# Optimization experiments

Hardware: AMD Instinct MI355X
Metric: run time of the kernel (lower is better)

Reference implementation:

```python
import jax, jax.numpy as jnp
import numpy as np

B, S, D = 4, 1024, 4096
HQ, HKV, HD = 32, 8, 128
N_REP = HQ // HKV


def _rope(x, cos, sin):
    # x: [b, s, h, hd]; cos/sin: [s, hd//2]; pairs are (x[..., 2i], x[..., 2i+1])
    xr = x[..., 0::2]
    xi = x[..., 1::2]
    c = cos[None, :, None, :]
    s = sin[None, :, None, :]
    out_r = xr * c - xi * s
    out_i = xr * s + xi * c
    return jnp.stack([out_r, out_i], axis=-1).reshape(x.shape)


def setup_inputs() -> dict:
    key = jax.random.key(0)
    ks = jax.random.split(key, 6)
    x = jax.random.normal(ks[0], (B, S, D), dtype=jnp.float32)
    wq = jax.random.normal(ks[1], (HQ * HD, D), dtype=jnp.float32) * 0.02
    wk = jax.random.normal(ks[2], (HKV * HD, D), dtype=jnp.float32) * 0.02
    wv = jax.random.normal(ks[3], (HKV * HD, D), dtype=jnp.float32) * 0.02
    wo = jax.random.normal(ks[4], (D, HQ * HD), dtype=jnp.float32) * 0.02
    # standard rotary frequencies, theta=10000
    inv_freq = 1.0 / (10000.0 ** (np.arange(0, HD, 2, dtype=np.float32) / HD))
    angles = np.outer(np.arange(S, dtype=np.float32), inv_freq)  # [S, HD//2]
    freqs_cos = jnp.asarray(np.cos(angles), dtype=jnp.float32)
    freqs_sin = jnp.asarray(np.sin(angles), dtype=jnp.float32)
    cache_k = jnp.zeros((B, S, HKV, HD), dtype=jnp.float32)
    cache_v = jnp.zeros((B, S, HKV, HD), dtype=jnp.float32)
    return {"x": x, "wq": wq, "wk": wk, "wv": wv, "wo": wo,
            "freqs_cos": freqs_cos, "freqs_sin": freqs_sin,
            "cache_k": cache_k, "cache_v": cache_v, "start_pos": 0}


def reference(x, wq, wk, wv, wo, freqs_cos, freqs_sin, cache_k, cache_v, start_pos):
    b, s, _ = x.shape
    xq = jnp.einsum('bsd,od->bso', x, wq).reshape(b, s, HQ, HD)
    xk = jnp.einsum('bsd,od->bso', x, wk).reshape(b, s, HKV, HD)
    xv = jnp.einsum('bsd,od->bso', x, wv).reshape(b, s, HKV, HD)
    xq = _rope(xq, freqs_cos, freqs_sin)
    xk = _rope(xk, freqs_cos, freqs_sin)
    # KV-cache append (intended semantics: store keys/values)
    cache_k = jax.lax.dynamic_update_slice(cache_k, xk, (0, start_pos, 0, 0))
    cache_v = jax.lax.dynamic_update_slice(cache_v, xv, (0, start_pos, 0, 0))
    keys = cache_k[:, :start_pos + s]      # [b, kv, HKV, HD]
    values = cache_v[:, :start_pos + s]
    # GQA repeat_kv -> [b, kv, HQ, HD]
    keys = jnp.repeat(keys, N_REP, axis=2)
    values = jnp.repeat(values, N_REP, axis=2)
    scores = jnp.einsum('bqhd,bkhd->bhqk', xq, keys) / jnp.sqrt(jnp.float32(HD))
    probs = jax.nn.softmax(scores.astype(jnp.float32), axis=-1).astype(xq.dtype)
    out = jnp.einsum('bhqk,bkhd->bqhd', probs, values).reshape(b, s, HQ * HD)
    return jnp.einsum('bso,do->bsd', out, wo)
```

## Files before the change

kernel.cpp:

```cpp
#include <hip/hip_runtime.h>

typedef __bf16 bf16_t;
typedef __bf16 bf16x8 __attribute__((ext_vector_type(8)));
typedef __bf16 bf16x4 __attribute__((ext_vector_type(4)));
typedef float  f32x4  __attribute__((ext_vector_type(4)));
typedef short  s16x4  __attribute__((ext_vector_type(4)));

#define SEQ    1024
#define DMODEL 4096
#define NHQ    32
#define NHKV   8
#define HDIM   128

#define GLOAD_LDS16(g, l)                                                  \
    __builtin_amdgcn_global_load_lds(                                      \
        (const __attribute__((address_space(1))) unsigned int*)(g),        \
        (__attribute__((address_space(3))) unsigned int*)(l), 16, 0, 0)

__global__ __launch_bounds__(256)
void f2b(const float* __restrict__ in, bf16_t* __restrict__ out, int n8)
{
    int i = blockIdx.x * 256 + threadIdx.x;
    if (i >= n8) return;
    const float4* p = (const float4*)in + 2 * (size_t)i;
    float4 a = p[0], b = p[1];
    bf16x8 o;
    o[0] = (bf16_t)a.x; o[1] = (bf16_t)a.y; o[2] = (bf16_t)a.z; o[3] = (bf16_t)a.w;
    o[4] = (bf16_t)b.x; o[5] = (bf16_t)b.y; o[6] = (bf16_t)b.z; o[7] = (bf16_t)b.w;
    *((bf16x8*)out + i) = o;
}

#define STAGE_A(b, ks)  do {                                               \
    const char* as_ = Ab + (size_t)srow * Krb + (ks) + scol0;              \
    GLOAD_LDS16(as_,             ldsA[b] + t * 16);                        \
    GLOAD_LDS16(as_ + 128 * Krb, ldsA[b] + 8192 + t * 16);                 \
} while (0)
#define STAGE_B(b, ks)  do {                                               \
    const char* bs_ = Bb + (size_t)srow * Krb + (ks) + scol0;              \
    GLOAD_LDS16(bs_,             ldsB[b] + t * 16);                        \
    GLOAD_LDS16(bs_ + 128 * Krb, ldsB[b] + 8192 + t * 16);                 \
} while (0)
#define LDS_AT(buf, row, lg_) \
    (*(const bf16x8*)((buf) + (row) * 64 + (((lg_) * 16) ^ ((((row) >> 1) & 3) << 4))))

#define TILE(bufi, tno)  do {                                              \
    const int ks3_ = ((tno) + 3 < NT) ? ((tno) + 3) * 64 : 0;              \
      \
    bf16x8 af[8], bfr0, bfr1;                                              \
    _Pragma("unroll")                                                      \
    for (int m = 0; m < 8; ++m) {                                          \
        int row = wm * 128 + m * 16 + l15;                                 \
        af[m] = LDS_AT(ldsA[bufi], row, lg);                               \
    }                                                                      \
    { int rb = wn * 64 + l15;      bfr0 = LDS_AT(ldsB[bufi], rb, lg); }    \
    { int rb = wn * 64 + 16 + l15; bfr1 = LDS_AT(ldsB[bufi], rb, lg); }    \
    STAGE_A(((tno) + 3) & 3, ks3_);                                        \
    __builtin_amdgcn_sched_barrier(0);                                     \
    __builtin_amdgcn_s_barrier();                                          \
    asm volatile("s_waitcnt lgkmcnt(0)" ::: "memory");                     \
    __builtin_amdgcn_sched_barrier(0);                                     \
    __builtin_amdgcn_s_setprio(1);                                         \
    _Pragma("unroll")                                                      \
    for (int m = 0; m < 8; ++m) {                                          \
        acc[m][0] = __builtin_amdgcn_mfma_f32_16x16x32_bf16(af[m], bfr0, acc[m][0], 0, 0, 0); \
        acc[m][1] = __builtin_amdgcn_mfma_f32_16x16x32_bf16(af[m], bfr1, acc[m][1], 0, 0, 0); \
    }                                                                      \
    __builtin_amdgcn_s_setprio(0);                                         \
    __builtin_amdgcn_sched_barrier(0);                                     \
    __builtin_amdgcn_s_barrier();                                          \
       \
    { int rb = wn * 64 + 32 + l15; bfr0 = LDS_AT(ldsB[bufi], rb, lg); }    \
    { int rb = wn * 64 + 48 + l15; bfr1 = LDS_AT(ldsB[bufi], rb, lg); }    \
    STAGE_B(((tno) + 3) & 3, ks3_);                                        \
    __builtin_amdgcn_sched_barrier(0);                                     \
    __builtin_amdgcn_s_barrier();                                          \
    asm volatile("s_waitcnt lgkmcnt(0)" ::: "memory");                     \
    __builtin_amdgcn_sched_barrier(0);                                     \
    __builtin_amdgcn_s_setprio(1);                                         \
    _Pragma("unroll")                                                      \
    for (int m = 0; m < 8; ++m) {                                          \
        acc[m][2] = __builtin_amdgcn_mfma_f32_16x16x32_bf16(af[m], bfr0, acc[m][2], 0, 0, 0); \
        acc[m][3] = __builtin_amdgcn_mfma_f32_16x16x32_bf16(af[m], bfr1, acc[m][3], 0, 0, 0); \
    }                                                                      \
    __builtin_amdgcn_s_setprio(0);                                         \
    asm volatile("s_waitcnt vmcnt(8)" ::: "memory");                       \
    __builtin_amdgcn_sched_barrier(0);                                     \
    __builtin_amdgcn_s_barrier();                                          \
} while (0)

template<bool OUT_F32>
__global__ __launch_bounds__(512, 2)
void gemm256(const bf16_t* __restrict__ A, const bf16_t* __restrict__ B,
             void* __restrict__ Cv, int M, int N, int K, int nbn)
{
    __shared__ __align__(16) char ldsA[4][16384];
    __shared__ __align__(16) char ldsB[4][16384];

    const int nwg = gridDim.x;
    const int bid0 = blockIdx.x;
    const int bid = (bid0 & 7) * (nwg >> 3) + (bid0 >> 3);
    const int bm = bid / nbn, bn = bid % nbn;
    const int t = threadIdx.x;
    const int lane = t & 63, wid = t >> 6;
    const int wm = wid >> 2, wn = wid & 3;
    const int l15 = lane & 15, lg = lane >> 4;
    const int m0 = bm * 256, n0 = bn * 256;

    const int srow = t >> 2;
    const int scol0 = (((t & 3) ^ ((srow >> 1) & 3)) << 4);
    const int Krb = K * 2;
    const char* Ab = (const char*)A + (size_t)m0 * Krb;
    const char* Bb = (const char*)B + (size_t)n0 * Krb;

    const int NT = K >> 5;
    f32x4 acc[8][4] = {};

    STAGE_A(0, 0);   STAGE_B(0, 0);
    STAGE_A(1, 64);  STAGE_B(1, 64);
    STAGE_A(2, 128); STAGE_B(2, 128);
    asm volatile("s_waitcnt vmcnt(8)" ::: "memory");
    __builtin_amdgcn_sched_barrier(0);
    __builtin_amdgcn_s_barrier();

    for (int tt = 0; tt < NT; tt += 4) {
        TILE(0, tt + 0);
        TILE(1, tt + 1);
        TILE(2, tt + 2);
        TILE(3, tt + 3);
    }

    #pragma unroll
    for (int m = 0; m < 8; ++m) {
        int row0 = m0 + wm * 128 + m * 16 + lg * 4;
        #pragma unroll
        for (int n = 0; n < 4; ++n) {
            int col = n0 + wn * 64 + n * 16 + l15;
            #pragma unroll
            for (int i = 0; i < 4; ++i) {
                if constexpr (OUT_F32)
                    ((float*)Cv)[(size_t)(row0 + i) * N + col] = acc[m][n][i];
                else
                    ((bf16_t*)Cv)[(size_t)(row0 + i) * N + col] = (bf16_t)acc[m][n][i];
            }
        }
    }
}
#undef TILE
#undef LDS_AT
#undef STAGE_A
#undef STAGE_B

template<int MODE>
__global__ __launch_bounds__(256, 4)
void gemm_bt(const bf16_t* __restrict__ A, const bf16_t* __restrict__ B,
             void* __restrict__ Cv, bf16_t* __restrict__ Vt,
             int M, int N, int K, int nbn)
{
    __shared__ __align__(16) bf16_t lA[128 * 32];
    __shared__ __align__(16) bf16_t lB[128 * 32];

    const int nwg = gridDim.x;
    const int bid0 = blockIdx.x;
    const int bid = (bid0 & 7) * (nwg >> 3) + (bid0 >> 3);
    const int bm = bid / nbn, bn = bid % nbn;
    const int t = threadIdx.x;
    const int lane = t & 63, wid = t >> 6;
    const int wrow = (wid >> 1) * 64, wcol = (wid & 1) * 64;
    const int l15 = lane & 15, lg = lane >> 4;
    const int m0 = bm * 128, n0 = bn * 128;

    const int r0 = t >> 2, pos0 = (t & 3) * 8;
    const int r1 = r0 + 64;

    const bf16_t* Ar0 = A + (size_t)(m0 + r0) * K + pos0;
    const bf16_t* Ar1 = A + (size_t)(m0 + r1) * K + pos0;
    const bf16_t* Br0 = B + (size_t)(n0 + r0) * K + pos0;
    const bf16_t* Br1 = B + (size_t)(n0 + r1) * K + pos0;

    f32x4 acc[4][4] = {};

    for (int k0 = 0; k0 < K; k0 += 32) {
        __syncthreads();
        GLOAD_LDS16(Ar0 + k0, lA + t * 8);
        GLOAD_LDS16(Ar1 + k0, lA + (t + 256) * 8);
        GLOAD_LDS16(Br0 + k0, lB + t * 8);
        GLOAD_LDS16(Br1 + k0, lB + (t + 256) * 8);
        __syncthreads();

        bf16x8 af[4], bfr[4];
        #pragma unroll
        for (int m = 0; m < 4; ++m)
            af[m] = *(const bf16x8*)(lA + (wrow + m * 16 + l15) * 32 + lg * 8);
        #pragma unroll
        for (int n = 0; n < 4; ++n)
            bfr[n] = *(const bf16x8*)(lB + (wcol + n * 16 + l15) * 32 + lg * 8);
        #pragma unroll
        for (int m = 0; m < 4; ++m)
            #pragma unroll
            for (int n = 0; n < 4; ++n)
                acc[m][n] = __builtin_amdgcn_mfma_f32_16x16x32_bf16(
                    af[m], bfr[n], acc[m][n], 0, 0, 0);
    }

    #pragma unroll
    for (int m = 0; m < 4; ++m) {
        #pragma unroll
        for (int n = 0; n < 4; ++n) {
            int col  = n0 + wcol + n * 16 + l15;
            int row0 = m0 + wrow + m * 16 + lg * 4;
            if constexpr (MODE == 0) {
                #pragma unroll
                for (int i = 0; i < 4; ++i)
                    ((bf16_t*)Cv)[(size_t)(row0 + i) * N + col] = (bf16_t)acc[m][n][i];
            } else if constexpr (MODE == 1) {
                #pragma unroll
                for (int i = 0; i < 4; ++i)
                    ((float*)Cv)[(size_t)(row0 + i) * N + col] = acc[m][n][i];
            } else {
                if (col < 1024) {
                    #pragma unroll
                    for (int i = 0; i < 4; ++i)
                        ((bf16_t*)Cv)[(size_t)(row0 + i) * 1024 + col] = (bf16_t)acc[m][n][i];
                } else {
                    bf16x4 pk;
                    #pragma unroll
                    for (int i = 0; i < 4; ++i) pk[i] = (bf16_t)acc[m][n][i];
                    *(bf16x4*)(Vt + (size_t)(col - 1024) * 4096 + row0) = pk;
                }
            }
        }
    }
}

__global__ __launch_bounds__(256)
void rope_kernel(bf16_t* __restrict__ X, const float* __restrict__ fc,
                 const float* __restrict__ fs, int nheads, int rowstride)
{
    int idx = blockIdx.x * 256 + threadIdx.x;
    int j4 = idx & 15;
    int rest = idx >> 4;
    int h = rest % nheads;
    int tok = rest / nheads;
    int s = tok & (SEQ - 1);
    bf16_t* p = X + (size_t)tok * rowstride + h * HDIM + j4 * 8;
    bf16x8 v = *(const bf16x8*)p;
    float4 c  = *(const float4*)(fc + s * 64 + j4 * 4);
    float4 sn = *(const float4*)(fs + s * 64 + j4 * 4);
    bf16x8 o;
    o[0] = (bf16_t)((float)v[0] * c.x - (float)v[1] * sn.x);
    o[1] = (bf16_t)((float)v[0] * sn.x + (float)v[1] * c.x);
    o[2] = (bf16_t)((float)v[2] * c.y - (float)v[3] * sn.y);
    o[3] = (bf16_t)((float)v[2] * sn.y + (float)v[3] * c.y);
    o[4] = (bf16_t)((float)v[4] * c.z - (float)v[5] * sn.z);
    o[5] = (bf16_t)((float)v[4] * sn.z + (float)v[5] * c.z);
    o[6] = (bf16_t)((float)v[6] * c.w - (float)v[7] * sn.w);
    o[7] = (bf16_t)((float)v[6] * sn.w + (float)v[7] * c.w);
    *(bf16x8*)p = o;
}

__global__ __launch_bounds__(256, 4)
void attn_kernel(const bf16_t* __restrict__ Q, const bf16_t* __restrict__ Kg,
                 const bf16_t* __restrict__ Vtg, bf16_t* __restrict__ O)
{
    __shared__ __align__(16) char klds[64 * 256];
    __shared__ __align__(16) char vlds[128 * 128];

    const int nwg = gridDim.x;
    const int bid0 = blockIdx.x;
    const int blk = (bid0 & 7) * (nwg >> 3) + (bid0 >> 3);
    const int qt = blk & 15;
    const int bh = blk >> 4;
    const int b = bh >> 5, h = bh & 31, kv = h >> 2;
    const int t = threadIdx.x, lane = t & 63, wid = t >> 6;
    const int l15 = lane & 15, lg = lane >> 4;
    const int swzk = (l15 & 7) << 4;

    const float SCL = 0.08838834764831845f;
    const float L2E = 1.4426950408889634f;

    const int qrow = qt * 64 + wid * 16 + l15;
    const size_t qbase = (size_t)(b * SEQ + qrow) * DMODEL + h * HDIM;
    bf16x8 qf[4];
    #pragma unroll
    for (int dc = 0; dc < 4; ++dc)
        qf[dc] = *(const bf16x8*)(Q + qbase + dc * 32 + lg * 8);

    const char* kgb = (const char*)Kg + ((size_t)(b * SEQ) * 1024 + kv * HDIM) * 2;
    const char* vgb = (const char*)Vtg + ((size_t)(kv * HDIM) * 4096 + b * SEQ) * 2;

    f32x4 o[8] = {};
    float mrun = -3.0e38f, lrun = 0.f;

    for (int kt = 0; kt < 16; ++kt) {
        __syncthreads();
        #pragma unroll
        for (int i = 0; i < 4; ++i) {
            int idx = t + 256 * i;
            {
                int r = idx >> 4, cb = (idx & 15) << 4;
                const char* src = kgb + (size_t)(kt * 64 + r) * 2048
                                      + (cb ^ ((r & 7) << 4));
                GLOAD_LDS16(src, klds + idx * 16);
            }
            {
                int d = idx >> 3, cb = (idx & 7) << 4;
                const char* src = vgb + (size_t)d * 8192 + kt * 128
                                      + (cb ^ ((d & 7) << 4));
                GLOAD_LDS16(src, vlds + idx * 16);
            }
        }
        __syncthreads();

        f32x4 sacc[4] = {};
        #pragma unroll
        for (int kb = 0; kb < 4; ++kb) {
            const char* krow = klds + (kb * 16 + l15) * 256;
            #pragma unroll
            for (int dc = 0; dc < 4; ++dc) {
                bf16x8 kf = *(const bf16x8*)(krow + ((dc * 64 + lg * 16) ^ swzk));
                sacc[kb] = __builtin_amdgcn_mfma_f32_16x16x32_bf16(
                    kf, qf[dc], sacc[kb], 0, 0, 0);
            }
        }

        float sv[16];
        float mt = -3.0e38f;
        #pragma unroll
        for (int kb = 0; kb < 4; ++kb)
            #pragma unroll
            for (int i = 0; i < 4; ++i) {
                float s = sacc[kb][i] * SCL;
                sv[kb * 4 + i] = s;
                mt = fmaxf(mt, s);
            }
        mt = fmaxf(mt, __shfl_xor(mt, 16));
        mt = fmaxf(mt, __shfl_xor(mt, 32));
        float mnew = fmaxf(mrun, mt);
        float alpha = exp2f((mrun - mnew) * L2E);

        float ts = 0.f;
        s16x4 pf[4];
        #pragma unroll
        for (int kb = 0; kb < 4; ++kb)
            #pragma unroll
            for (int i = 0; i < 4; ++i) {
                float p = exp2f((sv[kb * 4 + i] - mnew) * L2E);
                ts += p;
                pf[kb][i] = (short)__builtin_bit_cast(unsigned short, (bf16_t)p);
            }
        ts += __shfl_xor(ts, 16);
        ts += __shfl_xor(ts, 32);
        lrun = lrun * alpha + ts;
        mrun = mnew;

        #pragma unroll
        for (int i = 0; i < 4; ++i) {
            float ai = __shfl(alpha, lg * 4 + i);
            #pragma unroll
            for (int db = 0; db < 8; ++db) o[db][i] *= ai;
        }

        #pragma unroll
        for (int kb = 0; kb < 4; ++kb)
            #pragma unroll
            for (int db = 0; db < 8; ++db) {
                int d = l15 + 16 * db;
                const char* va = vlds + d * 128 + ((kb * 32 + lg * 8) ^ swzk);
                s16x4 vf = *(const s16x4*)va;
                o[db] = __builtin_amdgcn_mfma_f32_16x16x16bf16_1k(
                    pf[kb], vf, o[db], 0, 0, 0);
            }
    }

    #pragma unroll
    for (int i = 0; i < 4; ++i) {
        float li = __shfl(lrun, lg * 4 + i);
        float inv = 1.0f / li;
        int row = b * SEQ + qt * 64 + wid * 16 + lg * 4 + i;
        #pragma unroll
        for (int db = 0; db < 8; ++db) {
            int col = h * HDIM + l15 + 16 * db;
            O[(size_t)row * DMODEL + col] = (bf16_t)(o[db][i] * inv);
        }
    }
}

extern "C" void kernel_launch(void* const* d_in, const int* in_sizes, int n_in,
                              void* d_out, int out_size, void* d_ws, size_t ws_size,
                              hipStream_t stream)
{
    const float* x  = (const float*)d_in[0];
    const float* wq = (const float*)d_in[1];
    const float* wk = (const float*)d_in[2];
    const float* wv = (const float*)d_in[3];
    const float* wo = (const float*)d_in[4];
    const float* fc = (const float*)d_in[5];
    const float* fs = (const float*)d_in[6];

    const size_t T = (size_t)4096;
    bf16_t* Qw   = (bf16_t*)d_ws;
    bf16_t* Kw2  = Qw   + T * 4096;
    bf16_t* Vt   = Kw2  + T * 1024;
    bf16_t* AO   = Vt   + T * 1024;
    bf16_t* xb   = AO   + T * 4096;
    bf16_t* wqb  = xb   + T * 4096;
    bf16_t* wkvb = wqb  + T * 4096;
    bf16_t* wob  = wkvb + T * 2048;

    f2b<<<8192, 256, 0, stream>>>(x,  xb,  4096 * 4096 / 8);
    f2b<<<8192, 256, 0, stream>>>(wq, wqb, 4096 * 4096 / 8);
    f2b<<<2048, 256, 0, stream>>>(wk, wkvb,                       1024 * 4096 / 8);
    f2b<<<2048, 256, 0, stream>>>(wv, wkvb + (size_t)1024 * 4096, 1024 * 4096 / 8);
    f2b<<<8192, 256, 0, stream>>>(wo, wob, 4096 * 4096 / 8);

    gemm256<false><<<256, 512, 0, stream>>>(xb, wqb, Qw, 4096, 4096, 4096, 16);
    gemm_bt<2><<<512, 256, 0, stream>>>(xb, wkvb, Kw2, Vt, 4096, 2048, 4096, 16);

    rope_kernel<<<8192, 256, 0, stream>>>(Qw,  fc, fs, NHQ,  4096);
    rope_kernel<<<2048, 256, 0, stream>>>(Kw2, fc, fs, NHKV, 1024);

    attn_kernel<<<2048, 256, 0, stream>>>(Qw, Kw2, Vt, AO);

    gemm256<true><<<256, 512, 0, stream>>>(AO, wob, d_out, 4096, 4096, 4096, 16);
}
```

Baseline: 563.9 us.

## Double-buffer GEMM LDS fragments in registers and cut barriers per K-tile

Restructures the bf16 MFMA GEMM main loop so each K-tile's A and B fragments are loaded from LDS into a second register set while the current tile's MFMAs run. The three barriers per tile become one, and both A and B global-to-LDS stages are issued together at the top of the tile. The vmcnt and lgkmcnt waits are retuned to match. The aim is to hide LDS read latency and remove synchronization stalls, at the cost of extra VGPRs for the second fragment set, which could pressure occupancy at 512 threads with 2 blocks per CU.

```diff
diff --git a/kernel.cpp b/kernel.cpp
--- a/kernel.cpp
+++ b/kernel.cpp
@@ -43,49 +43,32 @@
 #define LDS_AT(buf, row, lg_) \
     (*(const bf16x8*)((buf) + (row) * 64 + (((lg_) * 16) ^ ((((row) >> 1) & 3) << 4))))
 
-#define TILE(bufi, tno)  do {                                              \
+#define TILE(bufi, tno, AC, BC, AN, BN)  do {                              \
     const int ks3_ = ((tno) + 3 < NT) ? ((tno) + 3) * 64 : 0;              \
-      \
-    bf16x8 af[8], bfr0, bfr1;                                              \
+    __builtin_amdgcn_s_barrier();           \
+    __builtin_amdgcn_sched_barrier(0);                                     \
+    STAGE_A(((tno) + 3) & 3, ks3_);                                        \
+    STAGE_B(((tno) + 3) & 3, ks3_);                                        \
     _Pragma("unroll")                                                      \
-    for (int m = 0; m < 8; ++m) {                                          \
-        int row = wm * 128 + m * 16 + l15;                                 \
-        af[m] = LDS_AT(ldsA[bufi], row, lg);                               \
-    }                                                                      \
-    { int rb = wn * 64 + l15;      bfr0 = LDS_AT(ldsB[bufi], rb, lg); }    \
-    { int rb = wn * 64 + 16 + l15; bfr1 = LDS_AT(ldsB[bufi], rb, lg); }    \
-    STAGE_A(((tno) + 3) & 3, ks3_);                                        \
-    __builtin_amdgcn_sched_barrier(0);                                     \
-    __builtin_amdgcn_s_barrier();                                          \
-    asm volatile("s_waitcnt lgkmcnt(0)" ::: "memory");                     \
+    for (int m = 0; m < 8; ++m)                                            \
+        AN[m] = LDS_AT(ldsA[((bufi) + 1) & 3], wm * 128 + m * 16 + l15, lg); \
+    _Pragma("unroll")                                                      \
+    for (int n = 0; n < 4; ++n)                                            \
+        BN[n] = LDS_AT(ldsB[((bufi) + 1) & 3], wn * 64 + n * 16 + l15, lg); \
+    asm volatile("s_waitcnt lgkmcnt(12)" ::: "memory");   \
     __builtin_amdgcn_sched_barrier(0);                                     \
     __builtin_amdgcn_s_setprio(1);                                         \
     _Pragma("unroll")                                                      \
     for (int m = 0; m < 8; ++m) {                                          \
-        acc[m][0] = __builtin_amdgcn_mfma_f32_16x16x32_bf16(af[m], bfr0, acc[m][0], 0, 0, 0); \
-        acc[m][1] = __builtin_amdgcn_mfma_f32_16x16x32_bf16(af[m], bfr1, acc[m][1], 0, 0, 0); \
+        acc[m][0] = __builtin_amdgcn_mfma_f32_16x16x32_bf16(AC[m], BC[0], acc[m][0], 0, 0, 0); \
+        acc[m][1] = __builtin_amdgcn_mfma_f32_16x16x32_bf16(AC[m], BC[1], acc[m][1], 0, 0, 0); \
+        acc[m][2] = __builtin_amdgcn_mfma_f32_16x16x32_bf16(AC[m], BC[2], acc[m][2], 0, 0, 0); \
+        acc[m][3] = __builtin_amdgcn_mfma_f32_16x16x32_bf16(AC[m], BC[3], acc[m][3], 0, 0, 0); \
     }                                                                      \
     __builtin_amdgcn_s_setprio(0);                                         \
     __builtin_amdgcn_sched_barrier(0);                                     \
-    __builtin_amdgcn_s_barrier();                                          \
-       \
-    { int rb = wn * 64 + 32 + l15; bfr0 = LDS_AT(ldsB[bufi], rb, lg); }    \
-    { int rb = wn * 64 + 48 + l15; bfr1 = LDS_AT(ldsB[bufi], rb, lg); }    \
-    STAGE_B(((tno) + 3) & 3, ks3_);                                        \
+    asm volatile("s_waitcnt vmcnt(4)" ::: "memory");       \
     __builtin_amdgcn_sched_barrier(0);                                     \
-    __builtin_amdgcn_s_barrier();                                          \
-    asm volatile("s_waitcnt lgkmcnt(0)" ::: "memory");                     \
-    __builtin_amdgcn_sched_barrier(0);                                     \
-    __builtin_amdgcn_s_setprio(1);                                         \
-    _Pragma("unroll")                                                      \
-    for (int m = 0; m < 8; ++m) {                                          \
-        acc[m][2] = __builtin_amdgcn_mfma_f32_16x16x32_bf16(af[m], bfr0, acc[m][2], 0, 0, 0); \
-        acc[m][3] = __builtin_amdgcn_mfma_f32_16x16x32_bf16(af[m], bfr1, acc[m][3], 0, 0, 0); \
-    }                                                                      \
-    __builtin_amdgcn_s_setprio(0);                                         \
-    asm volatile("s_waitcnt vmcnt(8)" ::: "memory");                       \
-    __builtin_amdgcn_sched_barrier(0);                                     \
-    __builtin_amdgcn_s_barrier();                                          \
 } while (0)
 
 template<bool OUT_F32>
@@ -114,19 +97,27 @@
 
     const int NT = K >> 5;
     f32x4 acc[8][4] = {};
+    bf16x8 afA[8], bfA[4], afB[8], bfB[4];
 
     STAGE_A(0, 0);   STAGE_B(0, 0);
     STAGE_A(1, 64);  STAGE_B(1, 64);
     STAGE_A(2, 128); STAGE_B(2, 128);
-    asm volatile("s_waitcnt vmcnt(8)" ::: "memory");
+    asm volatile("s_waitcnt vmcnt(4)" ::: "memory");
     __builtin_amdgcn_sched_barrier(0);
     __builtin_amdgcn_s_barrier();
 
+    #pragma unroll
+    for (int m = 0; m < 8; ++m)
+        afA[m] = LDS_AT(ldsA[0], wm * 128 + m * 16 + l15, lg);
+    #pragma unroll
+    for (int n = 0; n < 4; ++n)
+        bfA[n] = LDS_AT(ldsB[0], wn * 64 + n * 16 + l15, lg);
+
     for (int tt = 0; tt < NT; tt += 4) {
-        TILE(0, tt + 0);
-        TILE(1, tt + 1);
-        TILE(2, tt + 2);
-        TILE(3, tt + 3);
+        TILE(0, tt + 0, afA, bfA, afB, bfB);
+        TILE(1, tt + 1, afB, bfB, afA, bfA);
+        TILE(2, tt + 2, afA, bfA, afB, bfB);
+        TILE(3, tt + 3, afB, bfB, afA, bfA);
     }
 
     #pragma unroll
```

New measurement: 577.4 us. 2.4% more time.
